# Optimization experiments

Measured on AMD Instinct MI355X. Metric: run time of the kernel, lower is better.

Reference implementation:

```python
import jax, jax.numpy as jnp
import numpy as np

N_EMBED = 1024
N_HEAD = 16
HEAD_DIM = N_EMBED // N_HEAD


def setup_inputs() -> dict:
    key = jax.random.key(0)
    ks = jax.random.split(key, 6)
    B, T, C = 4, 2048, N_EMBED
    scale = 1.0 / np.sqrt(C)
    x = jax.random.normal(ks[0], (B, T, C), dtype=jnp.float32)
    # torch nn.Linear weights are [out, in]; y = x @ W.T
    Wk = jax.random.normal(ks[1], (C, C), dtype=jnp.float32) * scale
    Wq = jax.random.normal(ks[2], (C, C), dtype=jnp.float32) * scale
    Wv = jax.random.normal(ks[3], (C, C), dtype=jnp.float32) * scale
    Wp = jax.random.normal(ks[4], (C, C), dtype=jnp.float32) * scale
    bp = jax.random.normal(ks[5], (C,), dtype=jnp.float32) * 0.01
    return {"x": x, "Wk": Wk, "Wq": Wq, "Wv": Wv, "Wp": Wp, "bp": bp}


def reference(x, Wk, Wq, Wv, Wp, bp):
    B, T, C = x.shape
    H, D = N_HEAD, HEAD_DIM
    # QKV projections (torch Linear: x @ W.T), split heads -> [B, H, T, D]
    k = (x @ Wk.T).reshape(B, T, H, D).transpose(0, 2, 1, 3)
    q = (x @ Wq.T).reshape(B, T, H, D).transpose(0, 2, 1, 3)
    v = (x @ Wv.T).reshape(B, T, H, D).transpose(0, 2, 1, 3)
    # scaled scores [B, H, T, T]
    att = jnp.einsum('bhtd,bhsd->bhts', q, k) * (1.0 / np.sqrt(D))
    causal = jnp.tril(jnp.ones((T, T), dtype=bool))
    att = jnp.where(causal[None, None, :, :], att, -jnp.inf)
    att = jax.nn.softmax(att, axis=-1)
    out = jnp.einsum('bhts,bhsd->bhtd', att, v)  # [B, H, T, D]
    out = out.transpose(0, 2, 1, 3).reshape(B, T, C)
    out = out @ Wp.T + bp
    return out
```

## Files before the change

kernel.cpp:

```cpp
#include <hip/hip_runtime.h>

typedef __bf16 bf16_t;
typedef bf16_t bf16x4 __attribute__((ext_vector_type(4)));
typedef bf16_t bf16x8 __attribute__((ext_vector_type(8)));
typedef float f32x4 __attribute__((ext_vector_type(4)));

#define B_ 4
#define T_ 2048
#define C_ 1024
#define H_ 16
#define D_ 64

#define GLDS(g, l)                                                          \
  __builtin_amdgcn_global_load_lds(                                         \
      (const __attribute__((address_space(1))) void*)(g),                   \
      (__attribute__((address_space(3))) void*)(l), 16, 0, 0)

static __device__ __forceinline__ f32x4 mfma16(bf16x8 a, bf16x8 b, f32x4 c) {
  return __builtin_amdgcn_mfma_f32_16x16x32_bf16(a, b, c, 0, 0, 0);
}

static __device__ __forceinline__ float exp2_hw(float x) {
  float r;
  asm("v_exp_f32 %0, %1" : "=v"(r) : "v"(x));
  return r;
}

__global__ void cvt_all(const float* __restrict__ x, const float* __restrict__ wq,
                        const float* __restrict__ wk, const float* __restrict__ wv,
                        const float* __restrict__ wp, bf16_t* __restrict__ xb,
                        bf16_t* __restrict__ wqb, bf16_t* __restrict__ wkb,
                        bf16_t* __restrict__ wvb, bf16_t* __restrict__ wpb) {
  int i = blockIdx.x * blockDim.x + threadIdx.x;
  const float* src;
  bf16_t* dst;
  int off;
  if (i < 2097152) {
    src = x; dst = xb; off = i;
  } else {
    int r = i - 2097152;
    int region = r >> 18;
    off = r & 262143;
    if (region == 0) { src = wq; dst = wqb; }
    else if (region == 1) { src = wk; dst = wkb; }
    else if (region == 2) { src = wv; dst = wvb; }
    else { src = wp; dst = wpb; }
  }
  float4 v = ((const float4*)src)[off];
  bf16x4 o = {(bf16_t)v.x, (bf16_t)v.y, (bf16_t)v.z, (bf16_t)v.w};
  ((bf16x4*)dst)[off] = o;
}

__global__ __launch_bounds__(512) void gemm_qkv(
    const bf16_t* __restrict__ xb, const bf16_t* __restrict__ wq,
    const bf16_t* __restrict__ wk, const bf16_t* __restrict__ wv,
    bf16_t* __restrict__ qo, bf16_t* __restrict__ ko, bf16_t* __restrict__ vt) {
  __shared__ bf16_t lA[128 * 64];
  __shared__ bf16_t lB[3][128 * 64];
  const int tid = threadIdx.x, wave = tid >> 6, lane = tid & 63;
  const int g = lane >> 4;
  const int bid = blockIdx.x;
  const int swz = ((bid & 7) << 6) | (bid >> 3);
  const int col0 = (swz & 7) * 128, row0 = (swz >> 3) * 128;
  const int wr = wave >> 2, wc = wave & 3;
  f32x4 acc[3][4][2] = {};
  for (int k0 = 0; k0 < C_; k0 += 64) {
#pragma unroll
    for (int i = 0; i < 2; ++i) {
      const int off = (i * 8 + wave) * 1024;
      const int lin = off + lane * 16;
      const int r = lin >> 7;
      const int c = ((lin >> 4) & 7) ^ (r & 7);
      GLDS(xb + (size_t)(row0 + r) * C_ + k0 + c * 8, lA + (off >> 1));
      GLDS(wq + (size_t)(col0 + r) * C_ + k0 + c * 8, &lB[0][off >> 1]);
      GLDS(wk + (size_t)(col0 + r) * C_ + k0 + c * 8, &lB[1][off >> 1]);
      GLDS(wv + (size_t)(col0 + r) * C_ + k0 + c * 8, &lB[2][off >> 1]);
    }
    __syncthreads();
#pragma unroll
    for (int s = 0; s < 2; ++s) {
      const int c = s * 4 + g;
      bf16x8 af[4];
#pragma unroll
      for (int m = 0; m < 4; ++m) {
        const int r = wr * 64 + m * 16 + (lane & 15);
        af[m] = *(const bf16x8*)((const char*)lA + r * 128 +
                                 ((c ^ (r & 7)) << 4));
      }
#pragma unroll
      for (int z = 0; z < 3; ++z) {
        bf16x8 bfr[2];
#pragma unroll
        for (int n = 0; n < 2; ++n) {
          const int r = wc * 32 + n * 16 + (lane & 15);
          bfr[n] = *(const bf16x8*)((const char*)lB[z] + r * 128 +
                                    ((c ^ (r & 7)) << 4));
        }
#pragma unroll
        for (int m = 0; m < 4; ++m)
#pragma unroll
          for (int n = 0; n < 2; ++n)
            acc[z][m][n] = mfma16(af[m], bfr[n], acc[z][m][n]);
      }
    }
    __syncthreads();
  }
#pragma unroll
  for (int z = 0; z < 3; ++z) {
    bf16_t* outb = (z == 0) ? qo : ((z == 1) ? ko : vt);
    const float qs = (z == 0) ? 0.125f * 1.4426950408889634f : 1.0f;
#pragma unroll
    for (int m = 0; m < 4; ++m) {
#pragma unroll
      for (int n = 0; n < 2; ++n) {
        const int gr = row0 + wr * 64 + m * 16 + ((lane >> 4) << 2);
        const int gc = col0 + wc * 32 + n * 16 + (lane & 15);
        const int b = gr >> 11, t = gr & (T_ - 1);
        const int h = gc >> 6, d = gc & 63;
        if (z < 2) {
#pragma unroll
          for (int j = 0; j < 4; ++j)
            outb[(((size_t)(b * H_ + h)) * T_ + (t + j)) * D_ + d] =
                (bf16_t)(acc[z][m][n][j] * qs);
        } else {
          bf16x4 pk = {(bf16_t)acc[z][m][n][0], (bf16_t)acc[z][m][n][1],
                       (bf16_t)acc[z][m][n][2], (bf16_t)acc[z][m][n][3]};
          *(bf16x4*)(outb + (((size_t)(b * H_ + h)) * D_ + d) * T_ + t) = pk;
        }
      }
    }
  }
}

__device__ __forceinline__ void gemm_mainloop(const bf16_t* __restrict__ A,
                                              const bf16_t* __restrict__ W,
                                              bf16_t* lA, bf16_t* lB, int row0,
                                              int col0, f32x4 (&acc)[4][4]) {
  const int tid = threadIdx.x;
  const int wave = tid >> 6, lane = tid & 63;
  const int wr = wave >> 1, wc = wave & 1;
  for (int k0 = 0; k0 < C_; k0 += 64) {
#pragma unroll
    for (int it = 0; it < 4; ++it) {
      const int off = (it * 4 + wave) * 1024;
      const int lin = off + lane * 16;
      const int r = lin >> 7;
      const int c = ((lin >> 4) & 7) ^ (r & 7);
      GLDS(A + (size_t)(row0 + r) * C_ + k0 + c * 8, lA + (off >> 1));
      GLDS(W + (size_t)(col0 + r) * C_ + k0 + c * 8, lB + (off >> 1));
    }
    __syncthreads();
#pragma unroll
    for (int s = 0; s < 2; ++s) {
      bf16x8 af[4], bfr[4];
#pragma unroll
      for (int m = 0; m < 4; ++m) {
        const int r = wr * 64 + m * 16 + (lane & 15);
        const int c = s * 4 + (lane >> 4);
        af[m] = *(const bf16x8*)((const char*)lA + r * 128 +
                                 ((c ^ (r & 7)) << 4));
      }
#pragma unroll
      for (int n = 0; n < 4; ++n) {
        const int r = wc * 64 + n * 16 + (lane & 15);
        const int c = s * 4 + (lane >> 4);
        bfr[n] = *(const bf16x8*)((const char*)lB + r * 128 +
                                  ((c ^ (r & 7)) << 4));
      }
#pragma unroll
      for (int m = 0; m < 4; ++m)
#pragma unroll
        for (int n = 0; n < 4; ++n) acc[m][n] = mfma16(af[m], bfr[n], acc[m][n]);
    }
    __syncthreads();
  }
}

__global__ __launch_bounds__(256) void gemm_proj(const bf16_t* __restrict__ att,
                                                 const bf16_t* __restrict__ wp,
                                                 const float* __restrict__ bias,
                                                 float* __restrict__ out) {
  __shared__ bf16_t lA[128 * 64];
  __shared__ bf16_t lB[128 * 64];
  const int row0 = blockIdx.y * 128, col0 = blockIdx.x * 128;
  f32x4 acc[4][4] = {};
  gemm_mainloop(att, wp, lA, lB, row0, col0, acc);
  const int lane = threadIdx.x & 63, wave = threadIdx.x >> 6;
  const int wr = wave >> 1, wc = wave & 1;
#pragma unroll
  for (int m = 0; m < 4; ++m) {
#pragma unroll
    for (int n = 0; n < 4; ++n) {
      const int gr = row0 + wr * 64 + m * 16 + ((lane >> 4) << 2);
      const int gc = col0 + wc * 64 + n * 16 + (lane & 15);
      const float bv = bias[gc];
#pragma unroll
      for (int j = 0; j < 4; ++j)
        out[(size_t)(gr + j) * C_ + gc] = acc[m][n][j] + bv;
    }
  }
}

__global__ __launch_bounds__(512, 4) void attn_fwd(
    const bf16_t* __restrict__ Q, const bf16_t* __restrict__ K,
    const bf16_t* __restrict__ V, bf16_t* __restrict__ AO) {
  __shared__ bf16_t lK[2][64 * 64];
  __shared__ bf16_t lV[2][64 * 64];
  __shared__ bf16_t lP[8][16 * 64];
  const int tid = threadIdx.x, wave = tid >> 6, lane = tid & 63;
  const int g = lane >> 4;
  const int bh = blockIdx.y;
  const size_t baseK = (size_t)bh * T_ * D_;
  const size_t baseV = (size_t)bh * D_ * T_;
  const int bb = bh >> 4, hh = bh & 15;

  int koff[2][4];
#pragma unroll
  for (int s = 0; s < 2; ++s)
#pragma unroll
    for (int nf = 0; nf < 4; ++nf) {
      const int r = nf * 16 + (lane & 15);
      const int c = s * 4 + g;
      koff[s][nf] = r * 128 + ((c ^ (r & 7)) << 4);
    }
  int pwoff[4];
  {
    const int r = lane & 15;
#pragma unroll
    for (int nf = 0; nf < 4; ++nf)
      pwoff[nf] = r * 128 + (((2 * nf + (g >> 1)) ^ (r & 7)) << 4) +
                  ((g & 1) << 3);
  }
  const int soff = wave * 1024;
  const int slin = soff + lane * 16;
  const int srow = slin >> 7;
  const int scol = ((slin >> 4) & 7) ^ (srow & 7);
  const size_t kgo = (size_t)srow * D_ + scol * 8;
  const size_t vgo = (size_t)srow * T_ + scol * 8;

  for (int half = 0; half < 2; ++half) {
    const int qt = half ? (15 - blockIdx.x) : blockIdx.x;
    const int twv = qt * 128 + wave * 16;
    const int ntiles = 2 * qt + 2;
    __syncthreads();
    GLDS(K + baseK + kgo, &lK[0][soff >> 1]);
    GLDS(V + baseV + vgo, &lV[0][soff >> 1]);
    bf16x8 qf[2];
#pragma unroll
    for (int s = 0; s < 2; ++s)
      qf[s] = *(const bf16x8*)(Q + baseK +
                               (size_t)(twv + (lane & 15)) * D_ + s * 32 +
                               (g << 3));
    float lrun = 0.f;
    f32x4 o[4] = {};
    int cur = 0;
    for (int it = 0; it < ntiles; ++it) {
      __syncthreads();
      if (it + 1 < ntiles) {
        const int nb = cur ^ 1;
        GLDS(K + baseK + (size_t)(it + 1) * 64 * D_ + kgo,
             &lK[nb][soff >> 1]);
        GLDS(V + baseV + (size_t)(it + 1) * 64 + vgo, &lV[nb][soff >> 1]);
      }
      const char* kb = (const char*)lK[cur];
      const char* vb = (const char*)lV[cur];
      const int s0 = it * 64;
      f32x4 sc[4];
#pragma unroll
      for (int nf = 0; nf < 4; ++nf) sc[nf] = (f32x4){};
      __builtin_amdgcn_s_setprio(1);
#pragma unroll
      for (int s = 0; s < 2; ++s)
#pragma unroll
        for (int nf = 0; nf < 4; ++nf)
          sc[nf] = mfma16(*(const bf16x8*)(kb + koff[s][nf]), qf[s], sc[nf]);
      __builtin_amdgcn_s_setprio(0);
      if (it >= 2 * qt) {
        const int t = twv + (lane & 15);
#pragma unroll
        for (int nf = 0; nf < 4; ++nf)
#pragma unroll
          for (int j = 0; j < 4; ++j) {
            const int s = s0 + nf * 16 + g * 4 + j;
            if (s > t) sc[nf][j] = -1e30f;
          }
      }
      bf16x4 pk[4];
      float psn[4];
#pragma unroll
      for (int nf = 0; nf < 4; ++nf) {
        float e0 = exp2_hw(sc[nf][0]);
        float e1 = exp2_hw(sc[nf][1]);
        float e2 = exp2_hw(sc[nf][2]);
        float e3 = exp2_hw(sc[nf][3]);
        pk[nf][0] = (bf16_t)e0;
        pk[nf][1] = (bf16_t)e1;
        pk[nf][2] = (bf16_t)e2;
        pk[nf][3] = (bf16_t)e3;
        psn[nf] = (e0 + e1) + (e2 + e3);
      }
      float ps = (psn[0] + psn[1]) + (psn[2] + psn[3]);
      ps += __shfl_xor(ps, 16);
      ps += __shfl_xor(ps, 32);
      lrun += ps;
      {
        char* pw = (char*)lP[wave];
#pragma unroll
        for (int nf = 0; nf < 4; ++nf) *(bf16x4*)(pw + pwoff[nf]) = pk[nf];
      }
      __builtin_amdgcn_s_setprio(1);
      const char* pb = (const char*)lP[wave];
#pragma unroll
      for (int s2 = 0; s2 < 2; ++s2) {
        bf16x8 pf = *(const bf16x8*)(pb + koff[s2][0]);
#pragma unroll
        for (int df = 0; df < 4; ++df)
          o[df] = mfma16(pf, *(const bf16x8*)(vb + koff[s2][df]), o[df]);
      }
      __builtin_amdgcn_s_setprio(0);
      cur ^= 1;
    }
    {
      const float inv = 1.0f / lrun;
      float ib[4];
#pragma unroll
      for (int j = 0; j < 4; ++j)
        ib[j] = __shfl(inv, (lane & 48) | ((g << 2) + j));
#pragma unroll
      for (int j = 0; j < 4; ++j) {
        const int t = twv + (g << 2) + j;
#pragma unroll
        for (int df = 0; df < 4; ++df) {
          const int cc = hh * 64 + df * 16 + (lane & 15);
          AO[((size_t)(bb * T_ + t)) * C_ + cc] = (bf16_t)(o[df][j] * ib[j]);
        }
      }
    }
  }
}

extern "C" void kernel_launch(void* const* d_in, const int* in_sizes, int n_in,
                              void* d_out, int out_size, void* d_ws,
                              size_t ws_size, hipStream_t stream) {
  const float* x = (const float*)d_in[0];
  const float* Wk = (const float*)d_in[1];
  const float* Wq = (const float*)d_in[2];
  const float* Wv = (const float*)d_in[3];
  const float* Wp = (const float*)d_in[4];
  const float* bp = (const float*)d_in[5];
  char* ws = (char*)d_ws;
  bf16_t* xb = (bf16_t*)ws;
  bf16_t* wqb = (bf16_t*)(ws + (16u << 20));
  bf16_t* wkb = (bf16_t*)(ws + (18u << 20));
  bf16_t* wvb = (bf16_t*)(ws + (20u << 20));
  bf16_t* wpb = (bf16_t*)(ws + (22u << 20));
  bf16_t* q = (bf16_t*)(ws + (24u << 20));
  bf16_t* k = (bf16_t*)(ws + (40u << 20));
  bf16_t* vt = (bf16_t*)(ws + (56u << 20));
  bf16_t* att = xb;

  cvt_all<<<12288, 256, 0, stream>>>(x, Wq, Wk, Wv, Wp, xb, wqb, wkb, wvb, wpb);
  gemm_qkv<<<512, 512, 0, stream>>>(xb, wqb, wkb, wvb, q, k, vt);
  attn_fwd<<<dim3(8, 64), 512, 0, stream>>>(q, k, vt, att);
  gemm_proj<<<dim3(8, 64), 256, 0, stream>>>(att, wpb, bp, (float*)d_out);
}
```

Measured before the change: 166.5 us.

## Double-buffer LDS tiles in QKV and projection GEMM mainloops

Both the QKV GEMM and the output-projection GEMM now keep two LDS stages. The next K-slice is prefetched with global_load_lds right after the barrier, while MFMAs run on the current slice, which leaves one barrier per iteration instead of two. Per-thread global offsets are precomputed once, outside the loop. This doubles shared-memory use (the QKV kernel goes to 128KB), which may cut how many blocks fit on each CU, in exchange for hiding global-load latency.

```diff
diff --git a/kernel.cpp b/kernel.cpp
--- a/kernel.cpp
+++ b/kernel.cpp
@@ -55,8 +55,8 @@
     const bf16_t* __restrict__ xb, const bf16_t* __restrict__ wq,
     const bf16_t* __restrict__ wk, const bf16_t* __restrict__ wv,
     bf16_t* __restrict__ qo, bf16_t* __restrict__ ko, bf16_t* __restrict__ vt) {
-  __shared__ bf16_t lA[128 * 64];
-  __shared__ bf16_t lB[3][128 * 64];
+  __shared__ bf16_t lA[2][128 * 64];
+  __shared__ bf16_t lB[2][3][128 * 64];
   const int tid = threadIdx.x, wave = tid >> 6, lane = tid & 63;
   const int g = lane >> 4;
   const int bid = blockIdx.x;
@@ -64,19 +64,32 @@
   const int col0 = (swz & 7) * 128, row0 = (swz >> 3) * 128;
   const int wr = wave >> 2, wc = wave & 3;
   f32x4 acc[3][4][2] = {};
+
+  const int soff[2] = {wave * 1024, (8 + wave) * 1024};
+  size_t sgo[2];
+#pragma unroll
+  for (int i = 0; i < 2; ++i) {
+    const int lin = soff[i] + lane * 16;
+    const int r = lin >> 7;
+    const int c = ((lin >> 4) & 7) ^ (r & 7);
+    sgo[i] = (size_t)r * C_ + c * 8;
+  }
+
+#define QKV_STAGE(k0, b)                                                    \
+  {                                                                         \
+    _Pragma("unroll") for (int i = 0; i < 2; ++i) {                         \
+      GLDS(xb + (size_t)row0 * C_ + (k0) + sgo[i], &lA[b][soff[i] >> 1]);   \
+      GLDS(wq + (size_t)col0 * C_ + (k0) + sgo[i], &lB[b][0][soff[i] >> 1]);\
+      GLDS(wk + (size_t)col0 * C_ + (k0) + sgo[i], &lB[b][1][soff[i] >> 1]);\
+      GLDS(wv + (size_t)col0 * C_ + (k0) + sgo[i], &lB[b][2][soff[i] >> 1]);\
+    }                                                                       \
+  }
+
+  QKV_STAGE(0, 0);
+  int cur = 0;
   for (int k0 = 0; k0 < C_; k0 += 64) {
-#pragma unroll
-    for (int i = 0; i < 2; ++i) {
-      const int off = (i * 8 + wave) * 1024;
-      const int lin = off + lane * 16;
-      const int r = lin >> 7;
-      const int c = ((lin >> 4) & 7) ^ (r & 7);
-      GLDS(xb + (size_t)(row0 + r) * C_ + k0 + c * 8, lA + (off >> 1));
-      GLDS(wq + (size_t)(col0 + r) * C_ + k0 + c * 8, &lB[0][off >> 1]);
-      GLDS(wk + (size_t)(col0 + r) * C_ + k0 + c * 8, &lB[1][off >> 1]);
-      GLDS(wv + (size_t)(col0 + r) * C_ + k0 + c * 8, &lB[2][off >> 1]);
-    }
     __syncthreads();
+    if (k0 + 64 < C_) QKV_STAGE(k0 + 64, cur ^ 1);
 #pragma unroll
     for (int s = 0; s < 2; ++s) {
       const int c = s * 4 + g;
@@ -84,7 +97,7 @@
 #pragma unroll
       for (int m = 0; m < 4; ++m) {
         const int r = wr * 64 + m * 16 + (lane & 15);
-        af[m] = *(const bf16x8*)((const char*)lA + r * 128 +
+        af[m] = *(const bf16x8*)((const char*)lA[cur] + r * 128 +
                                  ((c ^ (r & 7)) << 4));
       }
 #pragma unroll
@@ -93,7 +106,7 @@
 #pragma unroll
         for (int n = 0; n < 2; ++n) {
           const int r = wc * 32 + n * 16 + (lane & 15);
-          bfr[n] = *(const bf16x8*)((const char*)lB[z] + r * 128 +
+          bfr[n] = *(const bf16x8*)((const char*)lB[cur][z] + r * 128 +
                                     ((c ^ (r & 7)) << 4));
         }
 #pragma unroll
@@ -103,7 +116,7 @@
             acc[z][m][n] = mfma16(af[m], bfr[n], acc[z][m][n]);
       }
     }
-    __syncthreads();
+    cur ^= 1;
   }
 #pragma unroll
   for (int z = 0; z < 3; ++z) {
@@ -132,61 +145,66 @@
   }
 }
 
-__device__ __forceinline__ void gemm_mainloop(const bf16_t* __restrict__ A,
-                                              const bf16_t* __restrict__ W,
-                                              bf16_t* lA, bf16_t* lB, int row0,
-                                              int col0, f32x4 (&acc)[4][4]) {
-  const int tid = threadIdx.x;
-  const int wave = tid >> 6, lane = tid & 63;
-  const int wr = wave >> 1, wc = wave & 1;
-  for (int k0 = 0; k0 < C_; k0 += 64) {
-#pragma unroll
-    for (int it = 0; it < 4; ++it) {
-      const int off = (it * 4 + wave) * 1024;
-      const int lin = off + lane * 16;
-      const int r = lin >> 7;
-      const int c = ((lin >> 4) & 7) ^ (r & 7);
-      GLDS(A + (size_t)(row0 + r) * C_ + k0 + c * 8, lA + (off >> 1));
-      GLDS(W + (size_t)(col0 + r) * C_ + k0 + c * 8, lB + (off >> 1));
-    }
-    __syncthreads();
-#pragma unroll
-    for (int s = 0; s < 2; ++s) {
-      bf16x8 af[4], bfr[4];
-#pragma unroll
-      for (int m = 0; m < 4; ++m) {
-        const int r = wr * 64 + m * 16 + (lane & 15);
-        const int c = s * 4 + (lane >> 4);
-        af[m] = *(const bf16x8*)((const char*)lA + r * 128 +
-                                 ((c ^ (r & 7)) << 4));
-      }
-#pragma unroll
-      for (int n = 0; n < 4; ++n) {
-        const int r = wc * 64 + n * 16 + (lane & 15);
-        const int c = s * 4 + (lane >> 4);
-        bfr[n] = *(const bf16x8*)((const char*)lB + r * 128 +
-                                  ((c ^ (r & 7)) << 4));
-      }
-#pragma unroll
-      for (int m = 0; m < 4; ++m)
-#pragma unroll
-        for (int n = 0; n < 4; ++n) acc[m][n] = mfma16(af[m], bfr[n], acc[m][n]);
-    }
-    __syncthreads();
-  }
-}
-
 __global__ __launch_bounds__(256) void gemm_proj(const bf16_t* __restrict__ att,
                                                  const bf16_t* __restrict__ wp,
                                                  const float* __restrict__ bias,
                                                  float* __restrict__ out) {
-  __shared__ bf16_t lA[128 * 64];
-  __shared__ bf16_t lB[128 * 64];
+  __shared__ bf16_t lA[2][128 * 64];
+  __shared__ bf16_t lB[2][128 * 64];
+  const int tid = threadIdx.x;
+  const int wave = tid >> 6, lane = tid & 63;
+  const int wr = wave >> 1, wc = wave & 1;
   const int row0 = blockIdx.y * 128, col0 = blockIdx.x * 128;
   f32x4 acc[4][4] = {};
-  gemm_mainloop(att, wp, lA, lB, row0, col0, acc);
-  const int lane = threadIdx.x & 63, wave = threadIdx.x >> 6;
-  const int wr = wave >> 1, wc = wave & 1;
+
+  const int soff[4] = {wave * 1024, (4 + wave) * 1024, (8 + wave) * 1024,
+                       (12 + wave) * 1024};
+  size_t sgo[4];
+#pragma unroll
+  for (int i = 0; i < 4; ++i) {
+    const int lin = soff[i] + lane * 16;
+    const int r = lin >> 7;
+    const int c = ((lin >> 4) & 7) ^ (r & 7);
+    sgo[i] = (size_t)r * C_ + c * 8;
+  }
+
+#define PROJ_STAGE(k0, b)                                                   \
+  {                                                                         \
+    _Pragma("unroll") for (int i = 0; i < 4; ++i) {                         \
+      GLDS(att + (size_t)row0 * C_ + (k0) + sgo[i], &lA[b][soff[i] >> 1]);  \
+      GLDS(wp + (size_t)col0 * C_ + (k0) + sgo[i], &lB[b][soff[i] >> 1]);   \
+    }                                                                       \
+  }
+
+  PROJ_STAGE(0, 0);
+  int cur = 0;
+  for (int k0 = 0; k0 < C_; k0 += 64) {
+    __syncthreads();
+    if (k0 + 64 < C_) PROJ_STAGE(k0 + 64, cur ^ 1);
+#pragma unroll
+    for (int s = 0; s < 2; ++s) {
+      bf16x8 af[4], bfr[4];
+#pragma unroll
+      for (int m = 0; m < 4; ++m) {
+        const int r = wr * 64 + m * 16 + (lane & 15);
+        const int c = s * 4 + (lane >> 4);
+        af[m] = *(const bf16x8*)((const char*)lA[cur] + r * 128 +
+                                 ((c ^ (r & 7)) << 4));
+      }
+#pragma unroll
+      for (int n = 0; n < 4; ++n) {
+        const int r = wc * 64 + n * 16 + (lane & 15);
+        const int c = s * 4 + (lane >> 4);
+        bfr[n] = *(const bf16x8*)((const char*)lB[cur] + r * 128 +
+                                  ((c ^ (r & 7)) << 4));
+      }
+#pragma unroll
+      for (int m = 0; m < 4; ++m)
+#pragma unroll
+        for (int n = 0; n < 4; ++n) acc[m][n] = mfma16(af[m], bfr[n], acc[m][n]);
+    }
+    cur ^= 1;
+  }
 #pragma unroll
   for (int m = 0; m < 4; ++m) {
 #pragma unroll
```

After: 163.0 us. 2.1% less time.
